# Kernel optimization log

Hardware: AMD Instinct MI355X
Metric: run time of the kernel (lower is better)

The kernel has to match this reference:

```python
import jax, jax.numpy as jnp
import numpy as np

N, E = 50000, 250000          # nodes, edges
IN, OUT, EDIM = 9, 84, 1      # NNConv(9, 84), edge nn Linear(1, 9*84)
EPS = 1e-5                    # BatchNorm1d default eps


def setup_inputs() -> dict:
    key = jax.random.key(0)
    ks = jax.random.split(key, 8)
    return {
        "x": jax.random.normal(ks[0], (N, IN), jnp.float32),
        "edge_index": jax.random.randint(ks[1], (2, E), 0, N, dtype=jnp.int64),
        "edge_attr": jax.random.normal(ks[2], (E, EDIM), jnp.float32),
        # edge nn: Linear(EDIM, IN*OUT) generating per-edge weight matrices
        "nn_w": jax.random.normal(ks[3], (EDIM, IN * OUT), jnp.float32) * (1.0 / np.sqrt(EDIM)),
        "nn_b": jnp.zeros((IN * OUT,), jnp.float32),
        # NNConv root weight + bias
        "root": jax.random.normal(ks[4], (IN, OUT), jnp.float32) * (1.0 / np.sqrt(IN)),
        "bias": jnp.zeros((OUT,), jnp.float32),
        # BatchNorm1d(84) affine params
        "gamma": jnp.ones((OUT,), jnp.float32),
        "beta": jnp.zeros((OUT,), jnp.float32),
    }


def reference(x, edge_index, edge_attr, nn_w, nn_b, root, bias, gamma, beta):
    src, dst = edge_index[0], edge_index[1]
    # per-edge weight matrices: [E, IN, OUT]
    w_e = (edge_attr @ nn_w + nn_b).reshape(E, IN, OUT)
    # gather source node features and apply edge-specific matmul: [E, OUT]
    msg = jnp.einsum('ei,eio->eo', x[src], w_e)
    # scatter-add to destination nodes (NNConv default aggr='add'): [N, OUT]
    aggr = jax.ops.segment_sum(msg, dst, num_segments=N)
    out = x @ root + aggr + bias
    # BatchNorm1d(84), training mode (biased batch stats)
    mean = out.mean(0)
    var = out.var(0)
    out = (out - mean) * jax.lax.rsqrt(var + EPS) * gamma + beta
    return out
```

## Files before the change

kernel.cpp:

```cpp
#include <hip/hip_runtime.h>

#define N_NODES 50000
#define E_EDGES 250000
#define IN_F 9
#define OUT_F 84
#define GROUPS 21
#define BN_EPS 1e-5f

#define NB_TILE 48
#define NTILES ((N_NODES + NB_TILE - 1) / NB_TILE)
#define NCOPIES 32
#define CAP 32

#define VDIM 27
#define NPAIR 378
#define NM 405
#define SLEN 408

#define CNT_OFF   0
#define STATC_OFF 50048
#define SLOT_OFF  63232
#define S_OFF     3263232

__global__ void fill_slots_kernel(const int* __restrict__ ei,
                                  const float* __restrict__ ea,
                                  int* __restrict__ cnt,
                                  int2* __restrict__ slot,
                                  float* __restrict__ statc) {
    if (blockIdx.x == 0) {
        for (int t = threadIdx.x; t < NCOPIES * SLEN; t += blockDim.x)
            statc[t] = 0.0f;
    }
    int e = blockIdx.x * blockDim.x + threadIdx.x;
    if (e < E_EDGES) {
        int dst = ei[E_EDGES + e];
        int pos = atomicAdd(&cnt[dst], 1);
        if (pos < CAP)
            slot[dst * CAP + pos] = make_int2(ei[e], __float_as_int(ea[e]));
    }
}

__global__ void gather_gram_kernel(const float* __restrict__ x,
                                   const int*   __restrict__ cnt,
                                   const int2*  __restrict__ slot,
                                   float* __restrict__ S,
                                   float* __restrict__ statc) {
    __shared__ float V[VDIM * (NB_TILE + 1)];
    __shared__ __align__(16) int2 rec[NB_TILE][CAP];
    __shared__ int cnt_s[NB_TILE];
    __shared__ unsigned char pI[NPAIR], pJ[NPAIR];

    const int tid = threadIdx.x;
    const int nbase = blockIdx.x * NB_TILE;

    for (int t = tid; t < NPAIR; t += blockDim.x) {
        int tt = t, i = 0;
        while (tt >= VDIM - i) { tt -= VDIM - i; ++i; }
        pI[t] = (unsigned char)i;
        pJ[t] = (unsigned char)(i + tt);
    }
    if (tid < NB_TILE) {
        int n = nbase + tid;
        int c = (n < N_NODES) ? cnt[n] : 0;
        cnt_s[tid] = (c > CAP) ? CAP : c;
    }
    __syncthreads();

    if (tid < NB_TILE * 4) {
        int nl = tid >> 2, part = tid & 3;
        int c = cnt_s[nl];
        const int4* grow = (const int4*)&slot[(nbase + nl) * CAP];
        int4* lrow = (int4*)&rec[nl][0];
#pragma unroll
        for (int j = 0; j < 4; ++j) {
            int s = part * 8 + j * 2;
            if (s < c) lrow[part * 4 + j] = grow[part * 4 + j];
        }
    }
    __syncthreads();

    for (int it = tid; it < NB_TILE * IN_F; it += blockDim.x) {
        int nl = it / IN_F, i = it - nl * IN_F;
        int n = nbase + nl;
        float xv = 0.f, s0 = 0.f, s1 = 0.f;
        if (n < N_NODES) {
            xv = x[n * IN_F + i];
            int c = cnt_s[nl];
            const int2* r = rec[nl];
            int k = 0;
            for (; k + 4 <= c; k += 4) {
                int2 r0 = r[k], r1 = r[k+1], r2 = r[k+2], r3 = r[k+3];
                float a0 = x[r0.x * IN_F + i];
                float a1 = x[r1.x * IN_F + i];
                float a2 = x[r2.x * IN_F + i];
                float a3 = x[r3.x * IN_F + i];
                s0 += (a0 + a1) + (a2 + a3);
                s1 += __int_as_float(r0.y) * a0 + __int_as_float(r1.y) * a1
                    + __int_as_float(r2.y) * a2 + __int_as_float(r3.y) * a3;
            }
            for (; k < c; ++k) {
                int2 r0 = r[k];
                float a0 = x[r0.x * IN_F + i];
                s0 += a0;
                s1 += __int_as_float(r0.y) * a0;
            }
            S[n * 18 + i]     = s0;
            S[n * 18 + 9 + i] = s1;
        }
        V[i * (NB_TILE + 1) + nl]        = xv;
        V[(9 + i) * (NB_TILE + 1) + nl]  = s0;
        V[(18 + i) * (NB_TILE + 1) + nl] = s1;
    }
    __syncthreads();

    float* sc = statc + (blockIdx.x & (NCOPIES - 1)) * SLEN;
    for (int t = tid; t < NM; t += blockDim.x) {
        float acc = 0.f;
        if (t < NPAIR) {
            const float* vi = &V[pI[t] * (NB_TILE + 1)];
            const float* vj = &V[pJ[t] * (NB_TILE + 1)];
#pragma unroll
            for (int n = 0; n < NB_TILE; ++n) acc += vi[n] * vj[n];
        } else {
            const float* vi = &V[(t - NPAIR) * (NB_TILE + 1)];
#pragma unroll
            for (int n = 0; n < NB_TILE; ++n) acc += vi[n];
        }
        atomicAdd(&sc[t], acc);
    }
}

__global__ void final_kernel(const float* __restrict__ x,
                             const float* __restrict__ S,
                             const float* __restrict__ nw,
                             const float* __restrict__ nb,
                             const float* __restrict__ root,
                             const float* __restrict__ bias,
                             const float* __restrict__ gamma,
                             const float* __restrict__ beta,
                             const float* __restrict__ statc,
                             float* __restrict__ out) {
    __shared__ __align__(16) float4 Ws[IN_F * GROUPS];
    __shared__ __align__(16) float4 Bs[IN_F * GROUPS];
    __shared__ __align__(16) float4 Rs[IN_F * GROUPS];
    __shared__ __align__(16) float4 bs4[GROUPS];
    __shared__ float M[NM];
    __shared__ __align__(16) float scale[OUT_F];
    __shared__ __align__(16) float shift[OUT_F];
    __shared__ float Xt[NB_TILE * IN_F];
    __shared__ float St[NB_TILE * 18];

    const int tid = threadIdx.x;
    const int nbase = blockIdx.x * NB_TILE;

    for (int t = tid; t < IN_F * GROUPS; t += blockDim.x) {
        Ws[t] = ((const float4*)nw)[t];
        Bs[t] = ((const float4*)nb)[t];
        Rs[t] = ((const float4*)root)[t];
    }
    if (tid < GROUPS) bs4[tid] = ((const float4*)bias)[tid];

    for (int it = tid; it < NB_TILE * IN_F; it += blockDim.x) {
        int nl = it / IN_F, i = it - nl * IN_F;
        int n = nbase + nl;
        float xv = 0.f, s0 = 0.f, s1 = 0.f;
        if (n < N_NODES) {
            xv = x[n * IN_F + i];
            s0 = S[n * 18 + i];
            s1 = S[n * 18 + 9 + i];
        }
        Xt[nl * IN_F + i]   = xv;
        St[nl * 18 + i]     = s0;
        St[nl * 18 + 9 + i] = s1;
    }

    for (int t = tid; t < NM; t += blockDim.x) {
        float a = 0.f;
#pragma unroll
        for (int c = 0; c < NCOPIES; ++c) a += statc[c * SLEN + t];
        M[t] = a;
    }
    __syncthreads();

    if (tid < OUT_F) {
        const int o = tid, g4 = o >> 2, cm = o & 3;
        float c[VDIM];
#pragma unroll
        for (int i = 0; i < IN_F; ++i) {
            c[i]      = ((const float*)&Rs[i * GROUPS + g4])[cm];
            c[9 + i]  = ((const float*)&Bs[i * GROUPS + g4])[cm];
            c[18 + i] = ((const float*)&Ws[i * GROUPS + g4])[cm];
        }
        float sv = 0.f;
#pragma unroll
        for (int i = 0; i < VDIM; ++i) sv += M[NPAIR + i] * c[i];
        float q = 0.f;
        int t2 = 0;
        for (int i = 0; i < VDIM; ++i) {
            q += c[i] * c[i] * M[t2++];
            for (int j = i + 1; j < VDIM; ++j)
                q += 2.f * c[i] * c[j] * M[t2++];
        }
        const float b = ((const float*)&bs4[g4])[cm];
        const float inv_n = 1.0f / (float)N_NODES;
        float mean  = (sv + (float)N_NODES * b) * inv_n;
        float sumsq = q + 2.f * b * sv + (float)N_NODES * b * b;
        float var   = sumsq * inv_n - mean * mean;
        float sc    = rsqrtf(var + BN_EPS) * gamma[o];
        scale[o] = sc;
        shift[o] = beta[o] - mean * sc;
    }
    __syncthreads();

    const int g = tid % GROUPS;
    if (tid < 252) {
        float4 sc4 = *(const float4*)&scale[g * 4];
        float4 sh4 = *(const float4*)&shift[g * 4];
#pragma unroll
        for (int k = 0; k < 4; ++k) {
            int p  = tid + k * 252;
            int nl = p / GROUPS;
            int n  = nbase + nl;
            if (n < N_NODES) {
                float4 acc = bs4[g];
#pragma unroll
                for (int i = 0; i < IN_F; ++i) {
                    float xv = Xt[nl * IN_F + i];
                    float s0 = St[nl * 18 + i];
                    float s1 = St[nl * 18 + 9 + i];
                    float4 r = Rs[i * GROUPS + g];
                    float4 w = Ws[i * GROUPS + g];
                    float4 b = Bs[i * GROUPS + g];
                    acc.x += xv * r.x + s1 * w.x + s0 * b.x;
                    acc.y += xv * r.y + s1 * w.y + s0 * b.y;
                    acc.z += xv * r.z + s1 * w.z + s0 * b.z;
                    acc.w += xv * r.w + s1 * w.w + s0 * b.w;
                }
                acc.x = acc.x * sc4.x + sh4.x;
                acc.y = acc.y * sc4.y + sh4.y;
                acc.z = acc.z * sc4.z + sh4.z;
                acc.w = acc.w * sc4.w + sh4.w;
                *(float4*)&out[n * OUT_F + g * 4] = acc;
            }
        }
    }
}

extern "C" void kernel_launch(void* const* d_in, const int* in_sizes, int n_in,
                              void* d_out, int out_size, void* d_ws, size_t ws_size,
                              hipStream_t stream) {
    const float* x     = (const float*)d_in[0];
    const int*   ei    = (const int*)d_in[1];
    const float* ea    = (const float*)d_in[2];
    const float* nw    = (const float*)d_in[3];
    const float* nb    = (const float*)d_in[4];
    const float* root  = (const float*)d_in[5];
    const float* bias  = (const float*)d_in[6];
    const float* gamma = (const float*)d_in[7];
    const float* beta  = (const float*)d_in[8];
    float*       out   = (float*)d_out;

    float* wsf   = (float*)d_ws;
    int*   wsi   = (int*)d_ws;
    int*   cnt   = wsi + CNT_OFF;
    float* statc = wsf + STATC_OFF;
    int2*  slot  = (int2*)(wsi + SLOT_OFF);
    float* S     = wsf + S_OFF;

    hipMemsetAsync(cnt, 0, N_NODES * sizeof(int), stream);
    fill_slots_kernel<<<(E_EDGES + 255) / 256, 256, 0, stream>>>(ei, ea, cnt, slot, statc);
    gather_gram_kernel<<<NTILES, 256, 0, stream>>>(x, cnt, slot, S, statc);
    final_kernel<<<NTILES, 256, 0, stream>>>(x, S, nw, nb, root, bias,
                                             gamma, beta, statc, out);
}
```

Before: 122.2 us.

## Pre-gather source features into per-destination slot records during edge fill

The edge-fill kernel now reads each edge's source node features itself and writes them, with the edge attribute, as a 12-float record in the destination's slot row. The gather kernel then reads these contiguous records straight from global memory. This removes the shared-memory staging of index records and the dependent random gathers of x in the second kernel. In exchange it writes and reads much larger slot buffers (48 bytes per edge instead of 8) and moves the random x reads into the scattered fill kernel.

Measured after the change: 123.9 us. No clear change (+1.4%).

```diff
diff --git a/kernel.cpp b/kernel.cpp
--- a/kernel.cpp
+++ b/kernel.cpp
@@ -11,6 +11,7 @@
 #define NTILES ((N_NODES + NB_TILE - 1) / NB_TILE)
 #define NCOPIES 32
 #define CAP 32
+#define RECF 12
 
 #define VDIM 27
 #define NPAIR 378
@@ -20,12 +21,13 @@
 #define CNT_OFF   0
 #define STATC_OFF 50048
 #define SLOT_OFF  63232
-#define S_OFF     3263232
-
-__global__ void fill_slots_kernel(const int* __restrict__ ei,
+#define S_OFF     19263232
+
+__global__ void fill_slots_kernel(const float* __restrict__ x,
+                                  const int* __restrict__ ei,
                                   const float* __restrict__ ea,
                                   int* __restrict__ cnt,
-                                  int2* __restrict__ slot,
+                                  float* __restrict__ slot,
                                   float* __restrict__ statc) {
     if (blockIdx.x == 0) {
         for (int t = threadIdx.x; t < NCOPIES * SLEN; t += blockDim.x)
@@ -33,20 +35,29 @@
     }
     int e = blockIdx.x * blockDim.x + threadIdx.x;
     if (e < E_EDGES) {
-        int dst = ei[E_EDGES + e];
-        int pos = atomicAdd(&cnt[dst], 1);
-        if (pos < CAP)
-            slot[dst * CAP + pos] = make_int2(ei[e], __float_as_int(ea[e]));
+        int   src = ei[e];
+        int   dst = ei[E_EDGES + e];
+        float a   = ea[e];
+        int   pos = atomicAdd(&cnt[dst], 1);
+        if (pos < CAP) {
+            const float* xr = &x[src * IN_F];
+            float x0 = xr[0], x1 = xr[1], x2 = xr[2], x3 = xr[3];
+            float x4 = xr[4], x5 = xr[5], x6 = xr[6], x7 = xr[7];
+            float x8 = xr[8];
+            float4* r = (float4*)&slot[((long)dst * CAP + pos) * RECF];
+            r[0] = make_float4(x0, x1, x2, x3);
+            r[1] = make_float4(x4, x5, x6, x7);
+            r[2] = make_float4(x8, a, 0.f, 0.f);
+        }
     }
 }
 
 __global__ void gather_gram_kernel(const float* __restrict__ x,
                                    const int*   __restrict__ cnt,
-                                   const int2*  __restrict__ slot,
+                                   const float* __restrict__ slot,
                                    float* __restrict__ S,
                                    float* __restrict__ statc) {
     __shared__ float V[VDIM * (NB_TILE + 1)];
-    __shared__ __align__(16) int2 rec[NB_TILE][CAP];
     __shared__ int cnt_s[NB_TILE];
     __shared__ unsigned char pI[NPAIR], pJ[NPAIR];
 
@@ -63,19 +74,6 @@
         int n = nbase + tid;
         int c = (n < N_NODES) ? cnt[n] : 0;
         cnt_s[tid] = (c > CAP) ? CAP : c;
-    }
-    __syncthreads();
-
-    if (tid < NB_TILE * 4) {
-        int nl = tid >> 2, part = tid & 3;
-        int c = cnt_s[nl];
-        const int4* grow = (const int4*)&slot[(nbase + nl) * CAP];
-        int4* lrow = (int4*)&rec[nl][0];
-#pragma unroll
-        for (int j = 0; j < 4; ++j) {
-            int s = part * 8 + j * 2;
-            if (s < c) lrow[part * 4 + j] = grow[part * 4 + j];
-        }
     }
     __syncthreads();
 
@@ -86,23 +84,21 @@
         if (n < N_NODES) {
             xv = x[n * IN_F + i];
             int c = cnt_s[nl];
-            const int2* r = rec[nl];
+            const float* row = &slot[(long)n * CAP * RECF];
             int k = 0;
-            for (; k + 4 <= c; k += 4) {
-                int2 r0 = r[k], r1 = r[k+1], r2 = r[k+2], r3 = r[k+3];
-                float a0 = x[r0.x * IN_F + i];
-                float a1 = x[r1.x * IN_F + i];
-                float a2 = x[r2.x * IN_F + i];
-                float a3 = x[r3.x * IN_F + i];
-                s0 += (a0 + a1) + (a2 + a3);
-                s1 += __int_as_float(r0.y) * a0 + __int_as_float(r1.y) * a1
-                    + __int_as_float(r2.y) * a2 + __int_as_float(r3.y) * a3;
+            for (; k + 2 <= c; k += 2) {
+                float a0 = row[k * RECF + i];
+                float e0 = row[k * RECF + 9];
+                float a1 = row[(k + 1) * RECF + i];
+                float e1 = row[(k + 1) * RECF + 9];
+                s0 += a0 + a1;
+                s1 += e0 * a0 + e1 * a1;
             }
-            for (; k < c; ++k) {
-                int2 r0 = r[k];
-                float a0 = x[r0.x * IN_F + i];
+            if (k < c) {
+                float a0 = row[k * RECF + i];
+                float e0 = row[k * RECF + 9];
                 s0 += a0;
-                s1 += __int_as_float(r0.y) * a0;
+                s1 += e0 * a0;
             }
             S[n * 18 + i]     = s0;
             S[n * 18 + 9 + i] = s1;
@@ -264,11 +260,11 @@
     int*   wsi   = (int*)d_ws;
     int*   cnt   = wsi + CNT_OFF;
     float* statc = wsf + STATC_OFF;
-    int2*  slot  = (int2*)(wsi + SLOT_OFF);
+    float* slot  = wsf + SLOT_OFF;
     float* S     = wsf + S_OFF;
 
     hipMemsetAsync(cnt, 0, N_NODES * sizeof(int), stream);
-    fill_slots_kernel<<<(E_EDGES + 255) / 256, 256, 0, stream>>>(ei, ea, cnt, slot, statc);
+    fill_slots_kernel<<<(E_EDGES + 255) / 256, 256, 0, stream>>>(x, ei, ea, cnt, slot, statc);
     gather_gram_kernel<<<NTILES, 256, 0, stream>>>(x, cnt, slot, S, statc);
     final_kernel<<<NTILES, 256, 0, stream>>>(x, S, nw, nb, root, bias,
                                              gamma, beta, statc, out);
```
